# Optimization experiments

Hardware: AMD Instinct MI355X
Metric: run time of the kernel (lower is better)

Reference implementation:

```python
import jax, jax.numpy as jnp
import numpy as np

N, C, T, V = 64, 64, 300, 25  # batch, channels, frames, joints
CO = 64
EPS = 1e-5


def setup_inputs() -> dict:
    key = jax.random.key(0)
    ks = jax.random.split(key, 5)
    x = jax.random.normal(ks[0], (N, C, T, V), dtype=jnp.float32)
    lin_w = jax.random.normal(ks[1], (C, CO), dtype=jnp.float32) * np.sqrt(1.0 / CO)
    lin_b = jnp.zeros((1, 1, CO), dtype=jnp.float32)
    feat_mask = jax.random.normal(ks[2], (1, V, C), dtype=jnp.float32) * 0.1
    bn_gamma = jnp.ones((V * CO,), dtype=jnp.float32)
    bn_beta = jnp.zeros((V * CO,), dtype=jnp.float32)
    shift_in = jax.random.randint(ks[3], (V * C,), 0, V * C, dtype=jnp.int32)
    shift_out = jax.random.randint(ks[4], (V * CO,), 0, V * CO, dtype=jnp.int32)
    return {"x": x, "lin_w": lin_w, "lin_b": lin_b, "feat_mask": feat_mask,
            "bn_gamma": bn_gamma, "bn_beta": bn_beta,
            "shift_in": shift_in, "shift_out": shift_out}


def reference(x, lin_w, lin_b, feat_mask, bn_gamma, bn_beta, shift_in, shift_out):
    n, c, t, v = x.shape
    co = lin_w.shape[1]
    # (N,C,T,V) -> (N*T, V*C)
    xt = jnp.transpose(x, (0, 2, 3, 1)).reshape(n * t, v * c)
    # shift-in gather along feature axis
    xs = jnp.take(xt, shift_in, axis=1).reshape(n * t, v, c)
    # learned feature mask (tanh + 1)
    xs = xs * (jnp.tanh(feat_mask) + 1.0)
    # small channel-mixing matmul + bias
    y = jnp.einsum('nvc,cd->nvd', xs, lin_w) + lin_b  # (N*T, V, CO)
    y = y.reshape(n * t, v * co)
    # shift-out gather
    y = jnp.take(y, shift_out, axis=1)
    # BatchNorm1d (training mode: batch statistics over N*T)
    mean = jnp.mean(y, axis=0)
    var = jnp.mean(jnp.square(y - mean), axis=0)
    y = (y - mean) * jax.lax.rsqrt(var + EPS) * bn_gamma + bn_beta
    # back to (N, CO, T, V), residual (in==out -> identity down), ReLU
    y = jnp.transpose(y.reshape(n, t, v, co), (0, 3, 1, 2))
    return jax.nn.relu(y + x)
```

## Files before the change

### kernel.cpp

```cpp
#include <hip/hip_runtime.h>

typedef __bf16 bf16x8 __attribute__((ext_vector_type(8)));
typedef float f32x4 __attribute__((ext_vector_type(4)));

#define TID ((int)threadIdx.x)

constexpr int Nn = 64, Cc = 64, Tt = 300, Vv = 25;
constexpr int Fin = 1600;
constexpr int RowsT = 19200;
constexpr int TBR = 16;
constexpr int NTB = 19;
constexpr int RAWE = Cc * TBR * Vv;
constexpr int YP = 21;
constexpr float EPSv = 1e-5f;

__device__ __forceinline__ unsigned short f2b(float f) {
  unsigned u = __float_as_uint(f);
  return (unsigned short)((u + 0x7fffu + ((u >> 16) & 1u)) >> 16);
}
__device__ __forceinline__ float b2f(unsigned short h) {
  return __uint_as_float(((unsigned)h) << 16);
}
__device__ __forceinline__ unsigned long long pack4(float a, float b, float c, float d) {
  return (unsigned long long)f2b(a)
       | ((unsigned long long)f2b(b) << 16)
       | ((unsigned long long)f2b(c) << 32)
       | ((unsigned long long)f2b(d) << 48);
}

__device__ __forceinline__ void stage_raw(const float* __restrict__ x,
                                          int n, int t0, int validg,
                                          unsigned short* raw) {
  const int base = n * 480000 + t0 * 25;
  if (validg == TBR * 25) {
    #pragma unroll
    for (int i = 0; i < 13; ++i) {
      int q = TID + i * 512;
      if (q < 6400) {
        int c = q / 100;
        int g4 = (q - c * 100) * 4;
        float4 xv = *reinterpret_cast<const float4*>(x + base + c * 7500 + g4);
        *reinterpret_cast<unsigned long long*>(raw + q * 4) = pack4(xv.x, xv.y, xv.z, xv.w);
      }
    }
  } else {
    #pragma unroll
    for (int i = 0; i < 13; ++i) {
      int q = TID + i * 512;
      if (q < 6400) {
        int c = q / 100;
        int g4 = (q - c * 100) * 4;
        float4 xv = make_float4(0.f, 0.f, 0.f, 0.f);
        if (g4 < validg)
          xv = *reinterpret_cast<const float4*>(x + base + c * 7500 + g4);
        *reinterpret_cast<unsigned long long*>(raw + q * 4) = pack4(xv.x, xv.y, xv.z, xv.w);
      }
    }
  }
}

__device__ __forceinline__ void stage_bt(const float* __restrict__ lin_w,
                                         unsigned short* bT) {
  #pragma unroll
  for (int i = 0; i < 8; ++i) {
    int e = TID + i * 512;
    int c = e >> 6, d = e & 63;
    bT[d * 64 + (((c >> 3) ^ (d & 7)) * 8) + (c & 7)] = f2b(lin_w[e]);
  }
}

__device__ __forceinline__ void stage_combo(const float* __restrict__ feat_mask,
                                            const int* __restrict__ shift_in,
                                            unsigned* combo) {
  #pragma unroll
  for (int i = 0; i < 4; ++i) {
    int j = TID + i * 512;
    if (j < Fin) {
      int s = shift_in[j];
      unsigned off = (unsigned)((s & 63) * 400 + (s >> 6));
      float m = tanhf(feat_mask[j]) + 1.0f;
      combo[j] = (off << 16) | (unsigned)f2b(m);
    }
  }
}

__device__ __forceinline__ void load_bfr(const unsigned short* bT, bf16x8 bf[2][4]) {
  int l = TID & 63;
  int row = l & 15, grp = l >> 4;
  #pragma unroll
  for (int ks = 0; ks < 2; ++ks)
    #pragma unroll
    for (int nt = 0; nt < 4; ++nt) {
      int d = nt * 16 + row;
      int blk = (ks * 4 + grp) ^ (d & 7);
      bf[ks][nt] = *reinterpret_cast<const bf16x8*>(bT + d * 64 + blk * 8);
    }
}

__device__ __forceinline__ bf16x8 build_a(const unsigned short* raw, const unsigned* combo,
                                          int v, int ks) {
  int l = TID & 63;
  int t = l & 15, grp = l >> 4;
  int jb = v * 64 + ks * 32 + grp * 8;
  bf16x8 a;
  #pragma unroll
  for (int i = 0; i < 8; ++i) {
    unsigned cb = combo[jb + i];
    float m = __uint_as_float((cb & 0xffffu) << 16);
    float xv = b2f(raw[(cb >> 16) + t * 25]);
    a[i] = (__bf16)(xv * m);
  }
  return a;
}

__global__ __launch_bounds__(512, 4) void k_stats(
    const float* __restrict__ x, const float* __restrict__ lin_w,
    const float* __restrict__ feat_mask, const int* __restrict__ shift_in,
    float* __restrict__ wsum)
{
  __shared__ __align__(16) unsigned char smem[65792];
  unsigned short* raw   = reinterpret_cast<unsigned short*>(smem);
  unsigned short* bT    = reinterpret_cast<unsigned short*>(smem + 51200);
  unsigned*       combo = reinterpret_cast<unsigned*>(smem + 59392);

  int bid = blockIdx.x;
  int n = bid / NTB, tb = bid - n * NTB;
  int t0 = tb * TBR;
  int valid = min(TBR, Tt - t0);
  stage_raw(x, n, t0, valid * 25, raw);
  stage_bt(lin_w, bT);
  stage_combo(feat_mask, shift_in, combo);
  __syncthreads();

  bf16x8 bf[2][4];
  load_bfr(bT, bf);
  int w = TID >> 6, l = TID & 63;
  float* wsq = wsum + Fin;
  #pragma unroll
  for (int k = 0; k < 4; ++k) {
    int v = w + 8 * k;
    if (v < Vv) {
      bf16x8 a0 = build_a(raw, combo, v, 0);
      bf16x8 a1 = build_a(raw, combo, v, 1);
      #pragma unroll
      for (int nt = 0; nt < 4; ++nt) {
        f32x4 acc = {0.f, 0.f, 0.f, 0.f};
        acc = __builtin_amdgcn_mfma_f32_16x16x32_bf16(a0, bf[0][nt], acc, 0, 0, 0);
        acc = __builtin_amdgcn_mfma_f32_16x16x32_bf16(a1, bf[1][nt], acc, 0, 0, 0);
        float p = acc[0] + acc[1] + acc[2] + acc[3];
        float q = acc[0]*acc[0] + acc[1]*acc[1] + acc[2]*acc[2] + acc[3]*acc[3];
        p += __shfl_xor(p, 16); p += __shfl_xor(p, 32);
        q += __shfl_xor(q, 16); q += __shfl_xor(q, 32);
        if ((l & 48) == 0) {
          int col = v * 64 + nt * 16 + (l & 15);
          atomicAdd(&wsum[col], p);
          atomicAdd(&wsq[col], q);
        }
      }
    }
  }
}

__global__ void k_epi(const float* __restrict__ wsum, const float* __restrict__ gamma,
                      const float* __restrict__ beta, const int* __restrict__ shift_out,
                      unsigned long long* __restrict__ epi_g) {
  int k = blockIdx.x * 256 + TID;
  if (k >= Fin) return;
  int s2 = shift_out[k];
  float sm = wsum[s2] * (1.0f / RowsT);
  float sq = wsum[Fin + s2] * (1.0f / RowsT);
  float var = fmaxf(sq - sm * sm, 0.f);
  float rstd = rsqrtf(var + EPSv);
  float sc = gamma[k] * rstd;
  unsigned short offb = f2b(beta[k] - sm * sc);
  int d = k & 63, v = k >> 6;
  unsigned long long e = (unsigned long long)__float_as_uint(sc)
                       | ((unsigned long long)offb << 32)
                       | ((unsigned long long)(unsigned)(s2 * YP) << 48);
  epi_g[d * 25 + v] = e;
}

__global__ __launch_bounds__(512, 4) void k_main(
    const float* __restrict__ x, const float* __restrict__ lin_w,
    const float* __restrict__ feat_mask, const int* __restrict__ shift_in,
    const unsigned long long* __restrict__ epi_g, float* __restrict__ out)
{
  __shared__ __align__(16) unsigned char smem[80000];
  unsigned short* raw   = reinterpret_cast<unsigned short*>(smem);
  unsigned short* bT    = reinterpret_cast<unsigned short*>(smem + 51200);
  unsigned*       combo = reinterpret_cast<unsigned*>(smem + 59392);
  unsigned short* ylds  = reinterpret_cast<unsigned short*>(smem);
  unsigned long long* epi = reinterpret_cast<unsigned long long*>(smem + 67200);

  int bid = blockIdx.x;
  int n = bid / NTB, tb = bid - n * NTB;
  int t0 = tb * TBR;
  int valid = min(TBR, Tt - t0);
  int validg = valid * 25;

  stage_raw(x, n, t0, validg, raw);
  stage_bt(lin_w, bT);
  stage_combo(feat_mask, shift_in, combo);
  #pragma unroll
  for (int i = 0; i < 4; ++i) {
    int j = TID + i * 512;
    if (j < Fin) epi[j] = epi_g[j];
  }
  __syncthreads();

  bf16x8 bf[2][4];
  load_bfr(bT, bf);
  int w = TID >> 6, l = TID & 63, grp = l >> 4;
  bf16x8 areg[4][2];
  #pragma unroll
  for (int k = 0; k < 4; ++k) {
    int v = w + 8 * k;
    if (v < Vv) {
      areg[k][0] = build_a(raw, combo, v, 0);
      areg[k][1] = build_a(raw, combo, v, 1);
    }
  }
  __syncthreads();

  #pragma unroll
  for (int k = 0; k < 4; ++k) {
    int v = w + 8 * k;
    if (v < Vv) {
      #pragma unroll
      for (int nt = 0; nt < 4; ++nt) {
        f32x4 acc = {0.f, 0.f, 0.f, 0.f};
        acc = __builtin_amdgcn_mfma_f32_16x16x32_bf16(areg[k][0], bf[0][nt], acc, 0, 0, 0);
        acc = __builtin_amdgcn_mfma_f32_16x16x32_bf16(areg[k][1], bf[1][nt], acc, 0, 0, 0);
        int col = v * 64 + nt * 16 + (l & 15);
        int o = col * YP + grp * 4;
        #pragma unroll
        for (int j = 0; j < 4; ++j) ylds[o + j] = f2b(acc[j]);
      }
    }
  }
  __syncthreads();

  const int obase = n * 480000 + t0 * 25;
  #pragma unroll
  for (int it = 0; it < 13; ++it) {
    int g = TID + it * 512;
    if (g < 6400) {
      int d = g / 100;
      int f0 = (g - d * 100) * 4;
      if (f0 < validg) {
        const float4 xr = *reinterpret_cast<const float4*>(x + obase + d * 7500 + f0);
        float4 o;
        float* op = &o.x;
        const float* xp = &xr.x;
        #pragma unroll
        for (int e = 0; e < 4; ++e) {
          int f = f0 + e;
          int t = f / 25;
          int v = f - t * 25;
          unsigned long long ep = epi[d * 25 + v];
          float sc = __uint_as_float((unsigned)ep);
          float of = b2f((unsigned short)(ep >> 32));
          int s2o = (int)(ep >> 48);
          float y = b2f(ylds[s2o + t]);
          op[e] = fmaxf(fmaf(y, sc, of) + xp[e], 0.f);
        }
        *reinterpret_cast<float4*>(out + obase + d * 7500 + f0) = o;
      }
    }
  }
}

extern "C" void kernel_launch(void* const* d_in, const int* in_sizes, int n_in,
                              void* d_out, int out_size, void* d_ws, size_t ws_size,
                              hipStream_t stream) {
  (void)in_sizes; (void)n_in; (void)out_size; (void)ws_size;
  const float* x        = (const float*)d_in[0];
  const float* lin_w    = (const float*)d_in[1];
  const float* feat_mask= (const float*)d_in[3];
  const float* gamma    = (const float*)d_in[4];
  const float* beta     = (const float*)d_in[5];
  const int*   shift_in = (const int*)d_in[6];
  const int*   shift_out= (const int*)d_in[7];
  float* wsum = (float*)d_ws;
  unsigned long long* epi_g = (unsigned long long*)((char*)d_ws + 12800);

  hipMemsetAsync(d_ws, 0, 12800, stream);
  k_stats<<<Nn * NTB, 512, 0, stream>>>(x, lin_w, feat_mask, shift_in, wsum);
  k_epi  <<<7, 256, 0, stream>>>(wsum, gamma, beta, shift_out, epi_g);
  k_main <<<Nn * NTB, 512, 0, stream>>>(x, lin_w, feat_mask, shift_in, epi_g, (float*)d_out);
}
```

Baseline: 135.7 us.

## Fold feature mask into per-joint weights and restructure stats pipeline

A new prep kernel folds tanh(mask)+1 into per-joint bf16 weight fragments laid out for direct MFMA loads. It also precomputes the gather offsets and zeroes the stats buffer, replacing the memset. The stats kernel now processes two tiles per block, accumulates in registers, and spreads atomics over 8 replica buffers to reduce contention. The epilogue kernel is folded into k_main, which re-reduces the replicas per block. This removes per-block weight staging and per-element mask multiplies, at the cost of redundant stats reduction in every main block and B fragments read from global or L2 memory.

```diff
diff --git a/kernel.cpp b/kernel.cpp
--- a/kernel.cpp
+++ b/kernel.cpp
@@ -2,23 +2,30 @@
 
 typedef __bf16 bf16x8 __attribute__((ext_vector_type(8)));
 typedef float f32x4 __attribute__((ext_vector_type(4)));
+typedef unsigned short u16;
+typedef u16 u16x8 __attribute__((ext_vector_type(8)));
 
 #define TID ((int)threadIdx.x)
 
-constexpr int Nn = 64, Cc = 64, Tt = 300, Vv = 25;
+constexpr int Nn = 64, Tt = 300, Vv = 25;
 constexpr int Fin = 1600;
 constexpr int RowsT = 19200;
 constexpr int TBR = 16;
 constexpr int NTB = 19;
-constexpr int RAWE = Cc * TBR * Vv;
+constexpr int RAWE = 64 * TBR * Vv;
 constexpr int YP = 21;
+constexpr int NREP = 8;
+constexpr int SBLK = 608;
 constexpr float EPSv = 1e-5f;
 
-__device__ __forceinline__ unsigned short f2b(float f) {
+constexpr int WS_WV   = 102400;
+constexpr int WS_OFFS = 307200;
+
+__device__ __forceinline__ u16 f2b(float f) {
   unsigned u = __float_as_uint(f);
-  return (unsigned short)((u + 0x7fffu + ((u >> 16) & 1u)) >> 16);
-}
-__device__ __forceinline__ float b2f(unsigned short h) {
+  return (u16)((u + 0x7fffu + ((u >> 16) & 1u)) >> 16);
+}
+__device__ __forceinline__ float b2f(u16 h) {
   return __uint_as_float(((unsigned)h) << 16);
 }
 __device__ __forceinline__ unsigned long long pack4(float a, float b, float c, float d) {
@@ -29,8 +36,7 @@
 }
 
 __device__ __forceinline__ void stage_raw(const float* __restrict__ x,
-                                          int n, int t0, int validg,
-                                          unsigned short* raw) {
+                                          int n, int t0, int validg, u16* raw) {
   const int base = n * 480000 + t0 * 25;
   if (validg == TBR * 25) {
     #pragma unroll
@@ -59,165 +65,150 @@
   }
 }
 
-__device__ __forceinline__ void stage_bt(const float* __restrict__ lin_w,
-                                         unsigned short* bT) {
+__device__ __forceinline__ bf16x8 loadB(const u16* __restrict__ wv,
+                                        int v, int ks, int nt, int l) {
+  return *reinterpret_cast<const bf16x8*>(wv + ((((v * 2 + ks) * 4) + nt) << 9) + l * 8);
+}
+
+__device__ __forceinline__ bf16x8 build_a(const u16* raw, const u16* __restrict__ offs,
+                                          int v, int ks, int t, int grp) {
+  int jb = v * 64 + ks * 32 + grp * 8;
+  u16x8 o = *reinterpret_cast<const u16x8*>(offs + jb);
+  u16x8 a;
+  #pragma unroll
+  for (int i = 0; i < 8; ++i) a[i] = raw[(int)o[i] + t * 25];
+  return *reinterpret_cast<bf16x8*>(&a);
+}
+
+__global__ void k_wv(const float* __restrict__ lin_w, const float* __restrict__ feat_mask,
+                     const int* __restrict__ shift_in, float* __restrict__ wsum,
+                     u16* __restrict__ wv, u16* __restrict__ offs) {
+  int gid = blockIdx.x * 256 + TID;
+  wsum[gid] = 0.f;
+  wsum[gid + 12800] = 0.f;
+  if (gid < Fin) {
+    int s = shift_in[gid];
+    offs[gid] = (u16)((s & 63) * 400 + (s >> 6));
+  }
+  int v = blockIdx.x >> 1, ks = blockIdx.x & 1;
+  int nt = (TID >> 6) & 3, l = TID & 63;
+  int c0 = ks * 32 + (l >> 4) * 8;
+  int d = nt * 16 + (l & 15);
+  u16x8 o8;
   #pragma unroll
   for (int i = 0; i < 8; ++i) {
-    int e = TID + i * 512;
-    int c = e >> 6, d = e & 63;
-    bT[d * 64 + (((c >> 3) ^ (d & 7)) * 8) + (c & 7)] = f2b(lin_w[e]);
-  }
-}
-
-__device__ __forceinline__ void stage_combo(const float* __restrict__ feat_mask,
-                                            const int* __restrict__ shift_in,
-                                            unsigned* combo) {
+    int c = c0 + i;
+    float m = tanhf(feat_mask[v * 64 + c]) + 1.0f;
+    o8[i] = f2b(m * lin_w[c * 64 + d]);
+  }
+  *reinterpret_cast<u16x8*>(wv + ((((v * 2 + ks) * 4) + nt) << 9) + l * 8) = o8;
+}
+
+__global__ __launch_bounds__(512, 4) void k_stats(
+    const float* __restrict__ x, const u16* __restrict__ wv,
+    const u16* __restrict__ offs, float* __restrict__ wsum)
+{
+  __shared__ __align__(16) u16 raw[RAWE];
+  int bid = blockIdx.x;
+  int w = TID >> 6, l = TID & 63;
+  int t_lane = l & 15, grp = l >> 4;
+  float p[4][4] = {{0}}, q[4][4] = {{0}};
+
+  #pragma unroll
+  for (int half = 0; half < 2; ++half) {
+    int tile = bid + half * SBLK;
+    int n = tile / NTB, tb = tile - n * NTB;
+    int t0 = tb * TBR;
+    int validg = min(TBR, Tt - t0) * 25;
+    if (half) __syncthreads();
+    stage_raw(x, n, t0, validg, raw);
+    __syncthreads();
+    #pragma unroll
+    for (int k = 0; k < 4; ++k) {
+      int v = w + 8 * k;
+      if (v < Vv) {
+        bf16x8 a0 = build_a(raw, offs, v, 0, t_lane, grp);
+        bf16x8 a1 = build_a(raw, offs, v, 1, t_lane, grp);
+        #pragma unroll
+        for (int nt = 0; nt < 4; ++nt) {
+          f32x4 acc = {0.f, 0.f, 0.f, 0.f};
+          acc = __builtin_amdgcn_mfma_f32_16x16x32_bf16(a0, loadB(wv, v, 0, nt, l), acc, 0, 0, 0);
+          acc = __builtin_amdgcn_mfma_f32_16x16x32_bf16(a1, loadB(wv, v, 1, nt, l), acc, 0, 0, 0);
+          p[k][nt] += acc[0] + acc[1] + acc[2] + acc[3];
+          q[k][nt] += acc[0]*acc[0] + acc[1]*acc[1] + acc[2]*acc[2] + acc[3]*acc[3];
+        }
+      }
+    }
+  }
+  float* ws_r = wsum + (bid & (NREP - 1)) * 3200;
+  #pragma unroll
+  for (int k = 0; k < 4; ++k) {
+    int v = w + 8 * k;
+    if (v < Vv) {
+      #pragma unroll
+      for (int nt = 0; nt < 4; ++nt) {
+        float pp = p[k][nt], qq = q[k][nt];
+        pp += __shfl_xor(pp, 16); pp += __shfl_xor(pp, 32);
+        qq += __shfl_xor(qq, 16); qq += __shfl_xor(qq, 32);
+        if ((l & 48) == 0) {
+          int col = v * 64 + nt * 16 + (l & 15);
+          atomicAdd(&ws_r[col], pp);
+          atomicAdd(&ws_r[1600 + col], qq);
+        }
+      }
+    }
+  }
+}
+
+__global__ __launch_bounds__(512, 4) void k_main(
+    const float* __restrict__ x, const u16* __restrict__ wv,
+    const u16* __restrict__ offs, const float* __restrict__ wsum,
+    const float* __restrict__ gamma, const float* __restrict__ beta,
+    const int* __restrict__ shift_out, float* __restrict__ out)
+{
+  __shared__ __align__(16) unsigned char smem[80000];
+  u16* raw  = reinterpret_cast<u16*>(smem);
+  u16* ylds = reinterpret_cast<u16*>(smem);
+  unsigned long long* epi = reinterpret_cast<unsigned long long*>(smem + 67200);
+
+  int bid = blockIdx.x;
+  int n = bid / NTB, tb = bid - n * NTB;
+  int t0 = tb * TBR;
+  int validg = min(TBR, Tt - t0) * 25;
+
+  stage_raw(x, n, t0, validg, raw);
+
   #pragma unroll
   for (int i = 0; i < 4; ++i) {
     int j = TID + i * 512;
     if (j < Fin) {
-      int s = shift_in[j];
-      unsigned off = (unsigned)((s & 63) * 400 + (s >> 6));
-      float m = tanhf(feat_mask[j]) + 1.0f;
-      combo[j] = (off << 16) | (unsigned)f2b(m);
-    }
-  }
-}
-
-__device__ __forceinline__ void load_bfr(const unsigned short* bT, bf16x8 bf[2][4]) {
-  int l = TID & 63;
-  int row = l & 15, grp = l >> 4;
-  #pragma unroll
-  for (int ks = 0; ks < 2; ++ks)
-    #pragma unroll
-    for (int nt = 0; nt < 4; ++nt) {
-      int d = nt * 16 + row;
-      int blk = (ks * 4 + grp) ^ (d & 7);
-      bf[ks][nt] = *reinterpret_cast<const bf16x8*>(bT + d * 64 + blk * 8);
-    }
-}
-
-__device__ __forceinline__ bf16x8 build_a(const unsigned short* raw, const unsigned* combo,
-                                          int v, int ks) {
-  int l = TID & 63;
-  int t = l & 15, grp = l >> 4;
-  int jb = v * 64 + ks * 32 + grp * 8;
-  bf16x8 a;
-  #pragma unroll
-  for (int i = 0; i < 8; ++i) {
-    unsigned cb = combo[jb + i];
-    float m = __uint_as_float((cb & 0xffffu) << 16);
-    float xv = b2f(raw[(cb >> 16) + t * 25]);
-    a[i] = (__bf16)(xv * m);
-  }
-  return a;
-}
-
-__global__ __launch_bounds__(512, 4) void k_stats(
-    const float* __restrict__ x, const float* __restrict__ lin_w,
-    const float* __restrict__ feat_mask, const int* __restrict__ shift_in,
-    float* __restrict__ wsum)
-{
-  __shared__ __align__(16) unsigned char smem[65792];
-  unsigned short* raw   = reinterpret_cast<unsigned short*>(smem);
-  unsigned short* bT    = reinterpret_cast<unsigned short*>(smem + 51200);
-  unsigned*       combo = reinterpret_cast<unsigned*>(smem + 59392);
-
-  int bid = blockIdx.x;
-  int n = bid / NTB, tb = bid - n * NTB;
-  int t0 = tb * TBR;
-  int valid = min(TBR, Tt - t0);
-  stage_raw(x, n, t0, valid * 25, raw);
-  stage_bt(lin_w, bT);
-  stage_combo(feat_mask, shift_in, combo);
+      int s2 = shift_out[j];
+      float sm = 0.f, sq = 0.f;
+      #pragma unroll
+      for (int r = 0; r < NREP; ++r) {
+        sm += wsum[r * 3200 + s2];
+        sq += wsum[r * 3200 + 1600 + s2];
+      }
+      sm *= (1.0f / RowsT);
+      sq *= (1.0f / RowsT);
+      float rstd = rsqrtf(fmaxf(sq - sm * sm, 0.f) + EPSv);
+      float sc = gamma[j] * rstd;
+      int d = j & 63, v = j >> 6;
+      epi[d * 25 + v] = (unsigned long long)__float_as_uint(sc)
+                      | ((unsigned long long)f2b(beta[j] - sm * sc) << 32)
+                      | ((unsigned long long)(unsigned)(s2 * YP) << 48);
+    }
+  }
   __syncthreads();
 
-  bf16x8 bf[2][4];
-  load_bfr(bT, bf);
-  int w = TID >> 6, l = TID & 63;
-  float* wsq = wsum + Fin;
+  int w = TID >> 6, l = TID & 63, grp = l >> 4, t_lane = l & 15;
+  bf16x8 areg[4][2];
   #pragma unroll
   for (int k = 0; k < 4; ++k) {
     int v = w + 8 * k;
     if (v < Vv) {
-      bf16x8 a0 = build_a(raw, combo, v, 0);
-      bf16x8 a1 = build_a(raw, combo, v, 1);
-      #pragma unroll
-      for (int nt = 0; nt < 4; ++nt) {
-        f32x4 acc = {0.f, 0.f, 0.f, 0.f};
-        acc = __builtin_amdgcn_mfma_f32_16x16x32_bf16(a0, bf[0][nt], acc, 0, 0, 0);
-        acc = __builtin_amdgcn_mfma_f32_16x16x32_bf16(a1, bf[1][nt], acc, 0, 0, 0);
-        float p = acc[0] + acc[1] + acc[2] + acc[3];
-        float q = acc[0]*acc[0] + acc[1]*acc[1] + acc[2]*acc[2] + acc[3]*acc[3];
-        p += __shfl_xor(p, 16); p += __shfl_xor(p, 32);
-        q += __shfl_xor(q, 16); q += __shfl_xor(q, 32);
-        if ((l & 48) == 0) {
-          int col = v * 64 + nt * 16 + (l & 15);
-          atomicAdd(&wsum[col], p);
-          atomicAdd(&wsq[col], q);
-        }
-      }
-    }
-  }
-}
-
-__global__ void k_epi(const float* __restrict__ wsum, const float* __restrict__ gamma,
-                      const float* __restrict__ beta, const int* __restrict__ shift_out,
-                      unsigned long long* __restrict__ epi_g) {
-  int k = blockIdx.x * 256 + TID;
-  if (k >= Fin) return;
-  int s2 = shift_out[k];
-  float sm = wsum[s2] * (1.0f / RowsT);
-  float sq = wsum[Fin + s2] * (1.0f / RowsT);
-  float var = fmaxf(sq - sm * sm, 0.f);
-  float rstd = rsqrtf(var + EPSv);
-  float sc = gamma[k] * rstd;
-  unsigned short offb = f2b(beta[k] - sm * sc);
-  int d = k & 63, v = k >> 6;
-  unsigned long long e = (unsigned long long)__float_as_uint(sc)
-                       | ((unsigned long long)offb << 32)
-                       | ((unsigned long long)(unsigned)(s2 * YP) << 48);
-  epi_g[d * 25 + v] = e;
-}
-
-__global__ __launch_bounds__(512, 4) void k_main(
-    const float* __restrict__ x, const float* __restrict__ lin_w,
-    const float* __restrict__ feat_mask, const int* __restrict__ shift_in,
-    const unsigned long long* __restrict__ epi_g, float* __restrict__ out)
-{
-  __shared__ __align__(16) unsigned char smem[80000];
-  unsigned short* raw   = reinterpret_cast<unsigned short*>(smem);
-  unsigned short* bT    = reinterpret_cast<unsigned short*>(smem + 51200);
-  unsigned*       combo = reinterpret_cast<unsigned*>(smem + 59392);
-  unsigned short* ylds  = reinterpret_cast<unsigned short*>(smem);
-  unsigned long long* epi = reinterpret_cast<unsigned long long*>(smem + 67200);
-
-  int bid = blockIdx.x;
-  int n = bid / NTB, tb = bid - n * NTB;
-  int t0 = tb * TBR;
-  int valid = min(TBR, Tt - t0);
-  int validg = valid * 25;
-
-  stage_raw(x, n, t0, validg, raw);
-  stage_bt(lin_w, bT);
-  stage_combo(feat_mask, shift_in, combo);
-  #pragma unroll
-  for (int i = 0; i < 4; ++i) {
-    int j = TID + i * 512;
-    if (j < Fin) epi[j] = epi_g[j];
-  }
-  __syncthreads();
-
-  bf16x8 bf[2][4];
-  load_bfr(bT, bf);
-  int w = TID >> 6, l = TID & 63, grp = l >> 4;
-  bf16x8 areg[4][2];
-  #pragma unroll
-  for (int k = 0; k < 4; ++k) {
-    int v = w + 8 * k;
-    if (v < Vv) {
-      areg[k][0] = build_a(raw, combo, v, 0);
-      areg[k][1] = build_a(raw, combo, v, 1);
+      areg[k][0] = build_a(raw, offs, v, 0, t_lane, grp);
+      areg[k][1] = build_a(raw, offs, v, 1, t_lane, grp);
     }
   }
   __syncthreads();
@@ -229,10 +220,9 @@
       #pragma unroll
       for (int nt = 0; nt < 4; ++nt) {
         f32x4 acc = {0.f, 0.f, 0.f, 0.f};
-        acc = __builtin_amdgcn_mfma_f32_16x16x32_bf16(areg[k][0], bf[0][nt], acc, 0, 0, 0);
-        acc = __builtin_amdgcn_mfma_f32_16x16x32_bf16(areg[k][1], bf[1][nt], acc, 0, 0, 0);
-        int col = v * 64 + nt * 16 + (l & 15);
-        int o = col * YP + grp * 4;
+        acc = __builtin_amdgcn_mfma_f32_16x16x32_bf16(areg[k][0], loadB(wv, v, 0, nt, l), acc, 0, 0, 0);
+        acc = __builtin_amdgcn_mfma_f32_16x16x32_bf16(areg[k][1], loadB(wv, v, 1, nt, l), acc, 0, 0, 0);
+        int o = (v * 64 + nt * 16 + t_lane) * YP + grp * 4;
         #pragma unroll
         for (int j = 0; j < 4; ++j) ylds[o + j] = f2b(acc[j]);
       }
@@ -259,9 +249,8 @@
           int v = f - t * 25;
           unsigned long long ep = epi[d * 25 + v];
           float sc = __uint_as_float((unsigned)ep);
-          float of = b2f((unsigned short)(ep >> 32));
-          int s2o = (int)(ep >> 48);
-          float y = b2f(ylds[s2o + t]);
+          float of = b2f((u16)(ep >> 32));
+          float y = b2f(ylds[(int)(ep >> 48) + t]);
           op[e] = fmaxf(fmaf(y, sc, of) + xp[e], 0.f);
         }
         *reinterpret_cast<float4*>(out + obase + d * 7500 + f0) = o;
@@ -282,10 +271,11 @@
   const int*   shift_in = (const int*)d_in[6];
   const int*   shift_out= (const int*)d_in[7];
   float* wsum = (float*)d_ws;
-  unsigned long long* epi_g = (unsigned long long*)((char*)d_ws + 12800);
-
-  hipMemsetAsync(d_ws, 0, 12800, stream);
-  k_stats<<<Nn * NTB, 512, 0, stream>>>(x, lin_w, feat_mask, shift_in, wsum);
-  k_epi  <<<7, 256, 0, stream>>>(wsum, gamma, beta, shift_out, epi_g);
-  k_main <<<Nn * NTB, 512, 0, stream>>>(x, lin_w, feat_mask, shift_in, epi_g, (float*)d_out);
-}
+  u16*   wv   = (u16*)((char*)d_ws + WS_WV);
+  u16*   offs = (u16*)((char*)d_ws + WS_OFFS);
+
+  k_wv   <<<50, 256, 0, stream>>>(lin_w, feat_mask, shift_in, wsum, wv, offs);
+  k_stats<<<SBLK, 512, 0, stream>>>(x, wv, offs, wsum);
+  k_main <<<Nn * NTB, 512, 0, stream>>>(x, wv, offs, wsum, gamma, beta, shift_out,
+                                        (float*)d_out);
+}
```

Result: slower. 187.3 us (+38.0%).
